# Optimization experiments

Hardware: AMD Instinct MI355X
Metric: run time of the kernel (lower is better)

The kernel has to match this reference:

```python
import jax, jax.numpy as jnp
import numpy as np

B = 1024
IN_H, IN_W = 128, 128
KH, KW = 10, 10
SH, SW = 5, 5
PH, PW = 2, 2
HP, WP = IN_H + 2 * PH, IN_W + 2 * PW          # padded dims: 132, 132
NKH = (IN_H - KH + 2 * PH) // SH + 1            # 25
NKW = (IN_W - KW + 2 * PW) // SW + 1            # 25
NK = NKH * NKW                                  # 625


def _build_weight_matrix(kernel_weights):
    """kernel_weights: [NK, KH, KW] -> sparse-structured dense [HP*WP, NK].
    Faithful to LocallyConnected2dV2._create_weight_matrix, vectorized."""
    i = jnp.arange(NK)
    start_i = (i // NKW) * SH                   # [NK]
    start_j = (i % NKW) * SW                    # [NK]
    # flat row index for each (kernel, k, l) tap in padded image
    rows = ((start_i[:, None, None] + jnp.arange(KH)[None, :, None]) * WP
            + start_j[:, None, None] + jnp.arange(KW)[None, None, :])  # [NK,KH,KW]
    rows = rows.reshape(NK, KH * KW)
    cols = i[:, None]                           # [NK,1] broadcasts over taps
    W = jnp.zeros((HP * WP, NK), dtype=kernel_weights.dtype)
    return W.at[rows, cols].set(kernel_weights.reshape(NK, KH * KW))


def setup_inputs() -> dict:
    key = jax.random.key(0)
    kx, kw, kb = jax.random.split(key, 3)
    x = jax.random.normal(kx, (B, IN_H, IN_W), dtype=jnp.float32)
    kernel_weights = jax.random.normal(kw, (NK, KH, KW), dtype=jnp.float32)
    W = _build_weight_matrix(kernel_weights)    # [HP*WP, NK]
    bias = jax.random.normal(kb, (NKH, NKW), dtype=jnp.float32)
    return {"x": x, "W": W, "bias": bias}


def reference(x, W, bias):
    # zero-pad spatial dims, flatten, dense GEMM against sparse-structured W
    xp = jnp.pad(x, ((0, 0), (PH, PH), (PW, PW)))          # [B,HP,WP]
    xf = xp.reshape(x.shape[0], HP * WP)                   # [B,HP*WP]
    out = xf @ W                                           # [B,NK]
    out = out.reshape(x.shape[0], NKH, NKW)
    return out + bias
```

## Files before the change

kernel.cpp:

```cpp
#include <hip/hip_runtime.h>

constexpr int BATCH = 1024;
constexpr int H     = 128;
constexpr int Wd    = 128;
constexpr int WPAD  = 132;
constexpr int KH    = 10;
constexpr int KW    = 10;
constexpr int STR   = 5;
constexpr int NKH   = 25;
constexpr int NKW   = 25;
constexpr int NK    = NKH * NKW;
constexpr int KSZ   = KH * KW;

constexpr int IMGS  = 2;
constexpr int ITERS = 4;
constexpr int IPB   = IMGS * ITERS;
constexpr int GGRP  = BATCH / IPB;

__global__ void gather_weights(const float* __restrict__ W, float* __restrict__ wg) {
    int t = blockIdx.x * blockDim.x + threadIdx.x;
    if (t >= NK * KSZ) return;
    int k  = t / KSZ, i = t % KSZ;
    int di = i / KW,  dj = i % KW;
    int ki = k / NKW, kj = k % NKW;
    int row = (ki * STR + di) * WPAD + (kj * STR + dj);
    wg[t] = W[row * NK + k];
}

template <bool USE_WG>
__global__ __launch_bounds__(256)
void lc2d_kernel(const float* __restrict__ x,
                 const float* __restrict__ wg,
                 const float* __restrict__ Wfull,
                 const float* __restrict__ bias,
                 float* __restrict__ out) {
    __shared__ float xs[IMGS][KH][WPAD];
    __shared__ float part[IMGS][NKW * KH + 2];

    const int ki  = blockIdx.x % NKH;
    const int g   = blockIdx.x / NKH;
    const int tid = threadIdx.x;
    const int kj  = tid / KH;
    const int di  = tid % KH;

    float wr[KW];
    if (tid < NKW * KH) {
        const int k = ki * NKW + kj;
        if (USE_WG) {
#pragma unroll
            for (int dj = 0; dj < KW; ++dj)
                wr[dj] = wg[k * KSZ + di * KW + dj];
        } else {
#pragma unroll
            for (int dj = 0; dj < KW; ++dj) {
                int row = (ki * STR + di) * WPAD + (kj * STR + dj);
                wr[dj] = Wfull[row * NK + k];
            }
        }
    }
    float bia = 0.f;
    if (tid < IMGS * NKW) bia = bias[ki * NKW + tid % NKW];

    if (tid < IMGS * KH * 4) {
        const int img = tid / (KH * 4);
        const int j   = tid % (KH * 4);
        const int r   = j / 4, c = j % 4;
        xs[img][r][(c < 2) ? c : (128 + c)] = 0.f;
    }

    const int r0 = ki * STR - 2;

    for (int it = 0; it < ITERS; ++it) {
        const int b0 = g * IPB + it * IMGS;

        for (int i = tid; i < IMGS * KH * 32; i += 256) {
            const int img = i / (KH * 32);
            const int j   = i % (KH * 32);
            const int r   = j / 32, c4 = j % 32;
            const int rg  = r0 + r;
            float4 v = make_float4(0.f, 0.f, 0.f, 0.f);
            if (rg >= 0 && rg < H)
                v = reinterpret_cast<const float4*>(
                        x + (long)(b0 + img) * (H * Wd) + rg * Wd)[c4];
            float* dst = &xs[img][r][2 + c4 * 4];
            dst[0] = v.x; dst[1] = v.y; dst[2] = v.z; dst[3] = v.w;
        }
        __syncthreads();

        if (tid < NKW * KH) {
#pragma unroll
            for (int img = 0; img < IMGS; ++img) {
                float s = 0.f;
                const float* xr = &xs[img][di][kj * STR];
#pragma unroll
                for (int dj = 0; dj < KW; ++dj)
                    s += xr[dj] * wr[dj];
                part[img][tid] = s;
            }
        }
        __syncthreads();

        if (tid < IMGS * NKW) {
            const int img = tid / NKW, kj2 = tid % NKW;
            float s = 0.f;
#pragma unroll
            for (int j2 = 0; j2 < KH; ++j2)
                s += part[img][kj2 * KH + j2];
            out[(long)(b0 + img) * NK + ki * NKW + kj2] = s + bia;
        }
    }
}

extern "C" void kernel_launch(void* const* d_in, const int* in_sizes, int n_in,
                              void* d_out, int out_size, void* d_ws, size_t ws_size,
                              hipStream_t stream) {
    const float* x    = (const float*)d_in[0];
    const float* W    = (const float*)d_in[1];
    const float* bias = (const float*)d_in[2];
    float* out = (float*)d_out;

    const dim3 grid(NKH * GGRP);
    if (ws_size >= (size_t)NK * KSZ * sizeof(float)) {
        float* wg = (float*)d_ws;
        gather_weights<<<(NK * KSZ + 255) / 256, 256, 0, stream>>>(W, wg);
        lc2d_kernel<true><<<grid, 256, 0, stream>>>(x, wg, W, bias, out);
    } else {
        lc2d_kernel<false><<<grid, 256, 0, stream>>>(x, nullptr, W, bias, out);
    }
}
```

Baseline: 132.5 us.

## Rewrite locally-connected kernel with fp16 packed dot2 and per-thread full reductions

Replaces the fp32 kernel with one that converts the input rows to packed fp16 in shared memory and pads the weights into aligned 16-wide fp16 rows held in registers. Each thread computes one whole output with fdot2 instructions, which removes the partial-sum shared buffer and the second sync stage. Each block now handles 10 images once instead of looping over 2-image iterations. The fp16 input and weights lose precision, and 80 weight registers per thread may limit occupancy.

```diff
diff --git a/kernel.cpp b/kernel.cpp
--- a/kernel.cpp
+++ b/kernel.cpp
@@ -1,114 +1,130 @@
 #include <hip/hip_runtime.h>
 
-constexpr int BATCH = 1024;
-constexpr int H     = 128;
-constexpr int Wd    = 128;
-constexpr int WPAD  = 132;
-constexpr int KH    = 10;
-constexpr int KW    = 10;
-constexpr int STR   = 5;
-constexpr int NKH   = 25;
-constexpr int NKW   = 25;
-constexpr int NK    = NKH * NKW;
-constexpr int KSZ   = KH * KW;
+typedef _Float16 f16x2 __attribute__((ext_vector_type(2)));
+typedef __fp16  fp16x2 __attribute__((ext_vector_type(2)));
 
-constexpr int IMGS  = 2;
-constexpr int ITERS = 4;
-constexpr int IPB   = IMGS * ITERS;
-constexpr int GGRP  = BATCH / IPB;
+constexpr int NKH  = 25, NKW = 25, NK = 625;
+constexpr int WPAD = 132;
+constexpr int IMGS = 10;
+constexpr int NGRP = (1024 + IMGS - 1) / IMGS;
+constexpr int ROW_U2 = 34;
+constexpr int IMG_U2 = 342;
+constexpr int WPT  = 160;
 
-__global__ void gather_weights(const float* __restrict__ W, float* __restrict__ wg) {
-    int t = blockIdx.x * blockDim.x + threadIdx.x;
-    if (t >= NK * KSZ) return;
-    int k  = t / KSZ, i = t % KSZ;
-    int di = i / KW,  dj = i % KW;
+union U2H { unsigned int u; f16x2 h; fp16x2 p; };
+
+__global__ void gather_wp(const float* __restrict__ W, _Float16* __restrict__ wgp) {
+    int t = blockIdx.x * 256 + threadIdx.x;
+    if (t >= NK * WPT) return;
+    int k = t / WPT, rem = t % WPT;
+    int di = rem >> 4, p = rem & 15;
     int ki = k / NKW, kj = k % NKW;
-    int row = (ki * STR + di) * WPAD + (kj * STR + dj);
-    wg[t] = W[row * NK + k];
+    int o = (5 * kj + 2) & 3;
+    int j = p - o;
+    float val = 0.f;
+    if (j >= 0 && j < 10)
+        val = W[(size_t)((ki * 5 + di) * WPAD + kj * 5 + j) * NK + k];
+    wgp[t] = (_Float16)val;
+}
+
+__device__ __forceinline__ float dot2acc(unsigned int a, unsigned int b, float c) {
+    U2H ua, ub; ua.u = a; ub.u = b;
+#if __has_builtin(__builtin_amdgcn_fdot2)
+    return __builtin_amdgcn_fdot2(ua.h, ub.h, c, false);
+#else
+    return c + (float)ua.h.x * (float)ub.h.x + (float)ua.h.y * (float)ub.h.y;
+#endif
 }
 
 template <bool USE_WG>
-__global__ __launch_bounds__(256)
-void lc2d_kernel(const float* __restrict__ x,
-                 const float* __restrict__ wg,
-                 const float* __restrict__ Wfull,
-                 const float* __restrict__ bias,
-                 float* __restrict__ out) {
-    __shared__ float xs[IMGS][KH][WPAD];
-    __shared__ float part[IMGS][NKW * KH + 2];
+__global__ __launch_bounds__(256, 4)
+void lc2d_f16(const float* __restrict__ x, const _Float16* __restrict__ wgp,
+              const float* __restrict__ Wfull,
+              const float* __restrict__ bias, float* __restrict__ out) {
+    __shared__ uint2 xs2[IMGS * IMG_U2];
 
-    const int ki  = blockIdx.x % NKH;
-    const int g   = blockIdx.x / NKH;
+    const int bid = blockIdx.x;
+    const int ki  = bid % NKH;
+    const int grp = bid / NKH;
     const int tid = threadIdx.x;
-    const int kj  = tid / KH;
-    const int di  = tid % KH;
 
-    float wr[KW];
-    if (tid < NKW * KH) {
-        const int k = ki * NKW + kj;
+    const int r0 = ki * 5 - 2;
+    for (int i = tid; i < IMGS * 340; i += 256) {
+        const int im = i / 340, rem = i % 340;
+        const int r = rem / 34, q = rem % 34;
+        const int rg = r0 + r;
+        const int b  = grp * IMGS + im;
+        uint2 val = make_uint2(0u, 0u);
+        if (q >= 1 && q <= 32 && rg >= 0 && b < 1024) {
+            const float4 v = *reinterpret_cast<const float4*>(
+                x + ((size_t)b << 14) + (rg << 7) + ((q - 1) << 2));
+            U2H u0, u1;
+            u0.p = __builtin_amdgcn_cvt_pkrtz(v.x, v.y);
+            u1.p = __builtin_amdgcn_cvt_pkrtz(v.z, v.w);
+            val.x = u0.u; val.y = u1.u;
+        }
+        xs2[im * IMG_U2 + r * ROW_U2 + q] = val;
+    }
+
+    const bool active = tid < IMGS * NKW;
+    const int img = tid / NKW, kj = tid % NKW;
+    const int k = ki * NKW + kj;
+    unsigned int wv[80];
+    float bval = 0.f;
+    if (active) {
         if (USE_WG) {
+            const uint4* wp = reinterpret_cast<const uint4*>(wgp + (size_t)k * WPT);
 #pragma unroll
-            for (int dj = 0; dj < KW; ++dj)
-                wr[dj] = wg[k * KSZ + di * KW + dj];
+            for (int t4 = 0; t4 < 20; ++t4) {
+                uint4 u = wp[t4];
+                wv[4 * t4 + 0] = u.x; wv[4 * t4 + 1] = u.y;
+                wv[4 * t4 + 2] = u.z; wv[4 * t4 + 3] = u.w;
+            }
         } else {
+            const int o = (5 * kj + 2) & 3;
 #pragma unroll
-            for (int dj = 0; dj < KW; ++dj) {
-                int row = (ki * STR + di) * WPAD + (kj * STR + dj);
-                wr[dj] = Wfull[row * NK + k];
+            for (int di = 0; di < 10; ++di) {
+#pragma unroll
+                for (int m = 0; m < 8; ++m) {
+                    float f0 = 0.f, f1 = 0.f;
+                    int j0 = 2 * m - o, j1 = 2 * m + 1 - o;
+                    if (j0 >= 0 && j0 < 10)
+                        f0 = Wfull[(size_t)((ki * 5 + di) * WPAD + kj * 5 + j0) * NK + k];
+                    if (j1 >= 0 && j1 < 10)
+                        f1 = Wfull[(size_t)((ki * 5 + di) * WPAD + kj * 5 + j1) * NK + k];
+                    U2H u; u.p = __builtin_amdgcn_cvt_pkrtz(f0, f1);
+                    wv[di * 8 + m] = u.u;
+                }
             }
         }
+        bval = bias[k];
     }
-    float bia = 0.f;
-    if (tid < IMGS * NKW) bia = bias[ki * NKW + tid % NKW];
+    __syncthreads();
 
-    if (tid < IMGS * KH * 4) {
-        const int img = tid / (KH * 4);
-        const int j   = tid % (KH * 4);
-        const int r   = j / 4, c = j % 4;
-        xs[img][r][(c < 2) ? c : (128 + c)] = 0.f;
+    if (!active) return;
+
+    const int h0 = (5 * kj + 2) & ~3;
+    const uint2* base = xs2 + img * IMG_U2 + (h0 >> 2);
+    float acc = 0.f;
+#pragma unroll
+    for (int di = 0; di < 10; ++di) {
+        const uint2 a0 = base[di * ROW_U2 + 0];
+        const uint2 a1 = base[di * ROW_U2 + 1];
+        const uint2 a2 = base[di * ROW_U2 + 2];
+        const uint2 a3 = base[di * ROW_U2 + 3];
+        const unsigned int* w8 = &wv[di * 8];
+        acc = dot2acc(a0.x, w8[0], acc);
+        acc = dot2acc(a0.y, w8[1], acc);
+        acc = dot2acc(a1.x, w8[2], acc);
+        acc = dot2acc(a1.y, w8[3], acc);
+        acc = dot2acc(a2.x, w8[4], acc);
+        acc = dot2acc(a2.y, w8[5], acc);
+        acc = dot2acc(a3.x, w8[6], acc);
+        acc = dot2acc(a3.y, w8[7], acc);
     }
-
-    const int r0 = ki * STR - 2;
-
-    for (int it = 0; it < ITERS; ++it) {
-        const int b0 = g * IPB + it * IMGS;
-
-        for (int i = tid; i < IMGS * KH * 32; i += 256) {
-            const int img = i / (KH * 32);
-            const int j   = i % (KH * 32);
-            const int r   = j / 32, c4 = j % 32;
-            const int rg  = r0 + r;
-            float4 v = make_float4(0.f, 0.f, 0.f, 0.f);
-            if (rg >= 0 && rg < H)
-                v = reinterpret_cast<const float4*>(
-                        x + (long)(b0 + img) * (H * Wd) + rg * Wd)[c4];
-            float* dst = &xs[img][r][2 + c4 * 4];
-            dst[0] = v.x; dst[1] = v.y; dst[2] = v.z; dst[3] = v.w;
-        }
-        __syncthreads();
-
-        if (tid < NKW * KH) {
-#pragma unroll
-            for (int img = 0; img < IMGS; ++img) {
-                float s = 0.f;
-                const float* xr = &xs[img][di][kj * STR];
-#pragma unroll
-                for (int dj = 0; dj < KW; ++dj)
-                    s += xr[dj] * wr[dj];
-                part[img][tid] = s;
-            }
-        }
-        __syncthreads();
-
-        if (tid < IMGS * NKW) {
-            const int img = tid / NKW, kj2 = tid % NKW;
-            float s = 0.f;
-#pragma unroll
-            for (int j2 = 0; j2 < KH; ++j2)
-                s += part[img][kj2 * KH + j2];
-            out[(long)(b0 + img) * NK + ki * NKW + kj2] = s + bia;
-        }
-    }
+    const int b = grp * IMGS + img;
+    if (b < 1024)
+        out[(size_t)b * NK + k] = acc + bval;
 }
 
 extern "C" void kernel_launch(void* const* d_in, const int* in_sizes, int n_in,
@@ -119,12 +135,12 @@
     const float* bias = (const float*)d_in[2];
     float* out = (float*)d_out;
 
-    const dim3 grid(NKH * GGRP);
-    if (ws_size >= (size_t)NK * KSZ * sizeof(float)) {
-        float* wg = (float*)d_ws;
-        gather_weights<<<(NK * KSZ + 255) / 256, 256, 0, stream>>>(W, wg);
-        lc2d_kernel<true><<<grid, 256, 0, stream>>>(x, wg, W, bias, out);
+    const dim3 grid(NKH * NGRP);
+    if (ws_size >= (size_t)NK * WPT * sizeof(_Float16)) {
+        _Float16* wgp = (_Float16*)d_ws;
+        gather_wp<<<(NK * WPT + 255) / 256, 256, 0, stream>>>(W, wgp);
+        lc2d_f16<true><<<grid, 256, 0, stream>>>(x, wgp, W, bias, out);
     } else {
-        lc2d_kernel<false><<<grid, 256, 0, stream>>>(x, nullptr, W, bias, out);
+        lc2d_f16<false><<<grid, 256, 0, stream>>>(x, nullptr, W, bias, out);
     }
 }
```

New measurement: 140.0 us. 1.06x slower.
